# Optimization experiments

Measured on AMD Instinct MI355X. Metric: run time of the kernel, lower is better.

Reference implementation:

```python
import jax, jax.numpy as jnp
import numpy as np

NUM_HEADS = 16
EPS = 1e-6  # LinearAttention.epsilon

def setup_inputs() -> dict:
    key = jax.random.key(0)
    ks = jax.random.split(key, 10)
    B, L, D = 4, 4096, 2048
    s = 1.0 / np.sqrt(D)
    x = jax.random.normal(ks[0], (B, L, D), dtype=jnp.float32)
    attention_mask = jnp.ones((B, L), dtype=jnp.float32)
    Wq = jax.random.normal(ks[1], (D, D), dtype=jnp.float32) * s
    bq = jnp.zeros((D,), dtype=jnp.float32)
    Wk = jax.random.normal(ks[2], (D, D), dtype=jnp.float32) * s
    bk = jnp.zeros((D,), dtype=jnp.float32)
    Wv = jax.random.normal(ks[3], (D, D), dtype=jnp.float32) * s
    bv = jnp.zeros((D,), dtype=jnp.float32)
    Wo = jax.random.normal(ks[4], (D, D), dtype=jnp.float32) * s
    bo = jnp.zeros((D,), dtype=jnp.float32)
    return {"x": x, "attention_mask": attention_mask, "Wq": Wq, "bq": bq,
            "Wk": Wk, "bk": bk, "Wv": Wv, "bv": bv, "Wo": Wo, "bo": bo}

def reference(x, attention_mask, Wq, bq, Wk, bk, Wv, bv, Wo, bo):
    B, L, Dm = x.shape
    H = NUM_HEADS
    Dh = Dm // H
    # q/k/v projections -> [B, H, L, Dh]
    def proj(W, b):
        return (x @ W + b).reshape(B, L, H, Dh).transpose(0, 2, 1, 3)
    q = proj(Wq, bq)
    k = proj(Wk, bk)
    v = proj(Wv, bv)
    # feature map: elu(x) + 1
    q = jax.nn.elu(q) + 1.0
    k = jax.nn.elu(k) + 1.0
    # mask keys/values: mask [B, 1, L, 1]
    m = attention_mask[:, None, :, None]
    k = k * m
    v = v * m
    # causal linear attention via cumulative sums over sequence dim
    k_cum = jnp.cumsum(k, axis=2)          # [B,H,L,Dh]
    kv_cum = jnp.cumsum(k * v, axis=2)     # [B,H,L,Dh] (diagonal kv state, as in source)
    z = jnp.sum(q * k_cum, axis=-1) + EPS  # [B,H,L]
    z = z * attention_mask[:, None, :]
    out = (q * kv_cum) / z[..., None]      # [B,H,L,Dh]
    out = out.transpose(0, 2, 1, 3).reshape(B, L, Dm)
    return out @ Wo + bo
```

## Files before the change

kernel.cpp:

```cpp
#include <hip/hip_runtime.h>
#include <cstdint>
#include <cstddef>

#define EPS_F 1e-6f

__device__ inline unsigned short f2bf(float f) {
    union { float f; unsigned u; } v; v.f = f;
    unsigned r = v.u + 0x7fffu + ((v.u >> 16) & 1u);
    return (unsigned short)(r >> 16);
}
__device__ inline float bf2f(unsigned u16) {
    union { unsigned u; float f; } v; v.u = u16 << 16; return v.f;
}

typedef __attribute__((ext_vector_type(8))) __bf16 bf16x8;
typedef __attribute__((ext_vector_type(8))) short short8;
typedef __attribute__((ext_vector_type(8))) unsigned short ushort8;
typedef __attribute__((ext_vector_type(4))) float floatx4;
typedef __attribute__((ext_vector_type(4))) unsigned uintx4;

__device__ inline void async_load16(const void* g, void* l) {
    __builtin_amdgcn_global_load_lds((const __attribute__((address_space(1))) void*)g,
                                     (__attribute__((address_space(3))) void*)l,
                                     16, 0, 0);
}

#define LDS_OFF(p) ((unsigned)(unsigned long long)(const __attribute__((address_space(3))) void*)(p))

__global__ void cast_x_kernel(const float* __restrict__ in, unsigned short* __restrict__ out, int n8) {
    int i = blockIdx.x * blockDim.x + threadIdx.x;
    if (i < n8) {
        float4 a = ((const float4*)in)[2 * i];
        float4 b = ((const float4*)in)[2 * i + 1];
        short8 o;
        o[0] = (short)f2bf(a.x); o[1] = (short)f2bf(a.y);
        o[2] = (short)f2bf(a.z); o[3] = (short)f2bf(a.w);
        o[4] = (short)f2bf(b.x); o[5] = (short)f2bf(b.y);
        o[6] = (short)f2bf(b.z); o[7] = (short)f2bf(b.w);
        ((short8*)out)[i] = o;
    }
}

__global__ void transpose_cast_kernel(const float* __restrict__ W0, const float* __restrict__ W1,
                                      const float* __restrict__ W2, const float* __restrict__ W3,
                                      unsigned short* __restrict__ WtBase, int n) {
    const float* W = (blockIdx.z == 0) ? W0 : (blockIdx.z == 1) ? W1 : (blockIdx.z == 2) ? W2 : W3;
    unsigned short* Wt = WtBase + (size_t)blockIdx.z * n * n;
    __shared__ float tile[32][33];
    int bx = blockIdx.x * 32;
    int by = blockIdx.y * 32;
    int tx = threadIdx.x;
    int ty = threadIdx.y;
    #pragma unroll
    for (int i = 0; i < 32; i += 8)
        tile[ty + i][tx] = W[(size_t)(by + ty + i) * n + bx + tx];
    __syncthreads();
    #pragma unroll
    for (int i = 0; i < 32; i += 8)
        Wt[(size_t)(bx + ty + i) * n + by + tx] = f2bf(tile[tx][ty + i]);
}

#define BMT 256
#define BNT 256
#define BKT 32
#define SLOT_ELEMS (BMT * BKT)
#define SLOT_BYTES 16384
#define DMODEL 2048

#define DSR(dst, base, OFF) \
    asm volatile("ds_read_b128 %0, %1 offset:" OFF : "=v"(dst) : "v"(base) : "memory")
#define READ_A0(f, base) { DSR(f[0], base, "0");    DSR(f[1], base, "1024"); \
                           DSR(f[2], base, "2048"); DSR(f[3], base, "3072"); }
#define READ_A1(f, base) { DSR(f[0], base, "4096"); DSR(f[1], base, "5120"); \
                           DSR(f[2], base, "6144"); DSR(f[3], base, "7168"); }
#define READ_B(f, base)  { DSR(f[0], base, "0");    DSR(f[1], base, "1024"); \
                           DSR(f[2], base, "2048"); DSR(f[3], base, "3072"); }

#define MFMA_HALF(i0, af, bf)                                                   \
    _Pragma("unroll")                                                           \
    for (int i_ = 0; i_ < 4; i_++) {                                            \
        bf16x8 a_ = __builtin_bit_cast(bf16x8, af[i_]);                         \
        _Pragma("unroll")                                                       \
        for (int j_ = 0; j_ < 4; j_++)                                          \
            acc[i0 + i_][j_] = __builtin_amdgcn_mfma_f32_16x16x32_bf16(         \
                a_, __builtin_bit_cast(bf16x8, bf[j_]), acc[i0 + i_][j_], 0, 0, 0); \
    }

#define GEMM_ITER(T, BCUR, BNXT)                                                \
  {                                                                             \
    const int T_ = (T);                                                         \
    if (T_ <= NT - 3)      asm volatile("s_waitcnt vmcnt(4)" ::: "memory");     \
    else if (T_ == NT - 2) asm volatile("s_waitcnt vmcnt(0)" ::: "memory");     \
    __builtin_amdgcn_s_barrier();                                               \
    __builtin_amdgcn_sched_barrier(0);                                          \
    if (T_ + 3 < NT) stage(T_ + 3, (T_ + 3) & 3);                               \
    asm volatile("s_waitcnt lgkmcnt(4)" ::: "memory");                          \
    __builtin_amdgcn_sched_barrier(0);                                          \
    __builtin_amdgcn_s_setprio(1);                                              \
    MFMA_HALF(0, af0, BCUR);                                                    \
    __builtin_amdgcn_s_setprio(0);                                              \
    const int tn_ = T_ + 1;                                                     \
    const unsigned aN_ = aLane + (unsigned)((tn_ & 3) * SLOT_BYTES);            \
    const unsigned bN_ = bLane + (unsigned)((tn_ & 3) * SLOT_BYTES);            \
    if (tn_ < NT) {                                                             \
      READ_A0(af0, aN_);                                                        \
      READ_B(BNXT, bN_);                                                        \
      asm volatile("s_waitcnt lgkmcnt(8)" ::: "memory");                        \
    } else {                                                                    \
      asm volatile("s_waitcnt lgkmcnt(0)" ::: "memory");                        \
    }                                                                           \
    __builtin_amdgcn_sched_barrier(0);                                          \
    __builtin_amdgcn_s_setprio(1);                                              \
    MFMA_HALF(4, af1, BCUR);                                                    \
    __builtin_amdgcn_s_setprio(0);                                              \
    if (tn_ < NT) { READ_A1(af1, aN_); }                                        \
  }

template<int FINAL>
__global__ __launch_bounds__(512, 2)
void gemm_kernel(const unsigned short* __restrict__ A,
                 const unsigned short* __restrict__ Bt,
                 const float* __restrict__ b0, const float* __restrict__ b1,
                 const float* __restrict__ b2,
                 const float* __restrict__ mask,
                 unsigned short* __restrict__ qo, unsigned short* __restrict__ ko,
                 unsigned short* __restrict__ vo,
                 float* __restrict__ Cf,
                 int M, int K) {
    __shared__ __align__(16) unsigned short As[4 * SLOT_ELEMS];
    __shared__ __align__(16) unsigned short Bs[4 * SLOT_ELEMS];

    const int tid  = threadIdx.x;
    const int lane = tid & 63;
    const int wave = tid >> 6;
    const int wr   = wave >> 2;
    const int wc   = wave & 3;
    const int quad  = lane >> 4;
    const int row16 = lane & 15;

    const int nwg = (int)(gridDim.x * gridDim.y);
    const int bid = (int)(blockIdx.y * gridDim.x + blockIdx.x);
    const int cpx = nwg >> 3;
    const int swz = (bid & 7) * cpx + (bid >> 3);
    const int bm  = swz % (int)gridDim.x;
    const int bn  = swz / (int)gridDim.x;

    const int m0    = bm * BMT;
    const int nglob = bn * BNT;
    int mat = 0, n0 = nglob;
    const float* bias = b0;
    unsigned short* Cb = nullptr;
    if (!FINAL) {
        mat  = nglob >> 11;
        n0   = nglob & (DMODEL - 1);
        bias = (mat == 0) ? b0 : (mat == 1) ? b1 : b2;
        Cb   = (mat == 0) ? qo : (mat == 1) ? ko : vo;
    }

    floatx4 acc[8][4] = {};

    const unsigned short* gA[2];
    const unsigned short* gB[2];
    #pragma unroll
    for (int b = 0; b < 2; b++) {
        int s = b * 512 + tid;
        int r = s >> 2, c = s & 3;
        int cg = c ^ ((r >> 1) & 3);
        gA[b] = A  + (size_t)(m0 + r) * K + cg * 8;
        gB[b] = Bt + (size_t)(nglob + r) * K + cg * 8;
    }

    const unsigned asB = LDS_OFF(As);
    const unsigned bsB = LDS_OFF(Bs);
    const unsigned cP    = (unsigned)(quad ^ ((row16 >> 1) & 3));
    const unsigned aLane = asB + (unsigned)(wr * 8192 + row16 * 64) + cP * 16u;
    const unsigned bLane = bsB + (unsigned)(wc * 4096 + row16 * 64) + cP * 16u;

    auto stage = [&](int tt, int sl) {
        const int koff = tt * BKT;
        #pragma unroll
        for (int b = 0; b < 2; b++) {
            int s = b * 512 + tid;
            async_load16(gA[b] + koff, As + sl * SLOT_ELEMS + s * 8);
            async_load16(gB[b] + koff, Bs + sl * SLOT_ELEMS + s * 8);
        }
    };

    const int NT = K / BKT;
    stage(0, 0); stage(1, 1); stage(2, 2);
    asm volatile("s_waitcnt vmcnt(8)" ::: "memory");
    __builtin_amdgcn_s_barrier();
    __builtin_amdgcn_sched_barrier(0);

    uintx4 af0[4], af1[4], bfE[4], bfO[4];
    READ_A0(af0, aLane);
    READ_B(bfE, bLane);
    READ_A1(af1, aLane);

    for (int t = 0; t < NT; t += 2) {
        GEMM_ITER(t,     bfE, bfO);
        GEMM_ITER(t + 1, bfO, bfE);
    }

    float bcache[4];
    #pragma unroll
    for (int j = 0; j < 4; j++) bcache[j] = bias[n0 + wc * 64 + j * 16 + row16];
    #pragma unroll
    for (int i = 0; i < 8; i++) {
        #pragma unroll
        for (int r = 0; r < 4; r++) {
            int row = m0 + wr * 128 + i * 16 + quad * 4 + r;
            float mr = 1.0f;
            if (!FINAL && mat >= 1) mr = mask[row];
            #pragma unroll
            for (int j = 0; j < 4; j++) {
                int col = n0 + wc * 64 + j * 16 + row16;
                float v = acc[i][j][r] + bcache[j];
                if (FINAL) {
                    Cf[(size_t)row * DMODEL + col] = v;
                } else {
                    if (mat <= 1) v = (v > 0.f) ? (v + 1.f) : __expf(v);
                    v *= mr;
                    Cb[(size_t)row * DMODEL + col] = f2bf(v);
                }
            }
        }
    }
}

#define SL    4096
#define SD    2048
#define SH    16
#define CHUNK 64
#define NCH   64

__global__ void scan_partial_kernel(const unsigned short* __restrict__ k,
                                    const unsigned short* __restrict__ v,
                                    float* __restrict__ sumK, float* __restrict__ sumKV) {
    int blk = blockIdx.x;
    int c = blk & (NCH - 1), bh = blk >> 6;
    int b = bh >> 4, h = bh & (SH - 1);
    int lane = threadIdx.x;
    int tg = lane >> 4, dg = lane & 15;
    size_t base = ((size_t)(b * SL + c * CHUNK + tg)) * SD + h * 128 + dg * 8;
    float sk[8] = {0.f, 0.f, 0.f, 0.f, 0.f, 0.f, 0.f, 0.f};
    float skv[8] = {0.f, 0.f, 0.f, 0.f, 0.f, 0.f, 0.f, 0.f};
    for (int it = 0; it < CHUNK / 4; it++) {
        ushort8 kw = *(const ushort8*)(k + base);
        ushort8 vw = *(const ushort8*)(v + base);
        #pragma unroll
        for (int j = 0; j < 8; j++) {
            float kf = bf2f(kw[j]);
            float vf = bf2f(vw[j]);
            sk[j] += kf; skv[j] += kf * vf;
        }
        base += (size_t)4 * SD;
    }
    #pragma unroll
    for (int j = 0; j < 8; j++) {
        sk[j]  += __shfl_xor(sk[j], 16);  sk[j]  += __shfl_xor(sk[j], 32);
        skv[j] += __shfl_xor(skv[j], 16); skv[j] += __shfl_xor(skv[j], 32);
    }
    if (tg == 0) {
        size_t o = ((size_t)bh * NCH + c) * 128 + dg * 8;
        *(float4*)(sumK  + o)     = make_float4(sk[0], sk[1], sk[2], sk[3]);
        *(float4*)(sumK  + o + 4) = make_float4(sk[4], sk[5], sk[6], sk[7]);
        *(float4*)(sumKV + o)     = make_float4(skv[0], skv[1], skv[2], skv[3]);
        *(float4*)(sumKV + o + 4) = make_float4(skv[4], skv[5], skv[6], skv[7]);
    }
}

__global__ void scan_offsets_kernel(const float* __restrict__ sumK, const float* __restrict__ sumKV,
                                    float* __restrict__ offK, float* __restrict__ offKV) {
    int bh = blockIdx.x;
    int d  = threadIdx.x;
    float aK = 0.f, aKV = 0.f;
    for (int c = 0; c < NCH; c++) {
        size_t o = ((size_t)bh * NCH + c) * 128 + d;
        float sk = sumK[o], skv = sumKV[o];
        offK[o] = aK; offKV[o] = aKV;
        aK += sk; aKV += skv;
    }
}

__global__ void scan_final_kernel(const unsigned short* __restrict__ q,
                                  const unsigned short* __restrict__ k,
                                  const unsigned short* __restrict__ v,
                                  const float* __restrict__ offK, const float* __restrict__ offKV,
                                  const float* __restrict__ mask,
                                  unsigned short* __restrict__ out) {
    int blk = blockIdx.x;
    int c = blk & (NCH - 1), bh = blk >> 6;
    int b = bh >> 4, h = bh & (SH - 1);
    int lane = threadIdx.x;
    size_t ob = ((size_t)bh * NCH + c) * 128 + 2 * lane;
    float2 kcv = *(const float2*)(offK  + ob);
    float2 kvv = *(const float2*)(offKV + ob);
    float kc0 = kcv.x, kc1 = kcv.y, kv0 = kvv.x, kv1 = kvv.y;
    size_t base = ((size_t)(b * SL + c * CHUNK)) * SD + h * 128 + 2 * lane;
    const float* mrow = mask + (size_t)b * SL + c * CHUNK;
    for (int s = 0; s < CHUNK / 4; s++) {
        unsigned kw[4], vw[4], qw[4];
        #pragma unroll
        for (int u = 0; u < 4; u++) {
            size_t a = base + (size_t)u * SD;
            kw[u] = *(const unsigned*)(k + a);
            vw[u] = *(const unsigned*)(v + a);
            qw[u] = *(const unsigned*)(q + a);
        }
        float p[4], n0[4], n1[4];
        #pragma unroll
        for (int u = 0; u < 4; u++) {
            float kk0 = bf2f(kw[u] & 0xffff), kk1 = bf2f(kw[u] >> 16);
            float vv0 = bf2f(vw[u] & 0xffff), vv1 = bf2f(vw[u] >> 16);
            float qq0 = bf2f(qw[u] & 0xffff), qq1 = bf2f(qw[u] >> 16);
            kc0 += kk0; kc1 += kk1;
            kv0 += kk0 * vv0; kv1 += kk1 * vv1;
            p[u]  = qq0 * kc0 + qq1 * kc1;
            n0[u] = qq0 * kv0; n1[u] = qq1 * kv1;
        }
        #pragma unroll
        for (int off = 32; off > 0; off >>= 1) {
            #pragma unroll
            for (int u = 0; u < 4; u++) p[u] += __shfl_xor(p[u], off);
        }
        #pragma unroll
        for (int u = 0; u < 4; u++) {
            float z = (p[u] + EPS_F) * mrow[s * 4 + u];
            float inv = 1.0f / z;
            unsigned o0 = f2bf(n0[u] * inv);
            unsigned o1 = f2bf(n1[u] * inv);
            *(unsigned*)(out + base + (size_t)u * SD) = o0 | (o1 << 16);
        }
        base += (size_t)4 * SD;
    }
}

extern "C" void kernel_launch(void* const* d_in, const int* in_sizes, int n_in,
                              void* d_out, int out_size, void* d_ws, size_t ws_size,
                              hipStream_t stream) {
    const float* x  = (const float*)d_in[0];
    const float* am = (const float*)d_in[1];
    const float* Wq = (const float*)d_in[2];
    const float* bq = (const float*)d_in[3];
    const float* Wk = (const float*)d_in[4];
    const float* bk = (const float*)d_in[5];
    const float* Wv = (const float*)d_in[6];
    const float* bv = (const float*)d_in[7];
    const float* Wo = (const float*)d_in[8];
    const float* bo = (const float*)d_in[9];
    float* out = (float*)d_out;

    const int Bb = 4, L = 4096, D = 2048;
    const int M = Bb * L;
    const size_t MD = (size_t)M * D;

    char* w = (char*)d_ws;
    unsigned short* xb    = (unsigned short*)w; w += MD * 2;
    unsigned short* qb    = (unsigned short*)w; w += MD * 2;
    unsigned short* kb    = (unsigned short*)w; w += MD * 2;
    unsigned short* vb    = (unsigned short*)w; w += MD * 2;
    unsigned short* WT    = (unsigned short*)w; w += (size_t)4 * D * D * 2;
    float* sumK  = (float*)w; w += (size_t)64 * NCH * 128 * 4;
    float* sumKV = (float*)w; w += (size_t)64 * NCH * 128 * 4;
    float* offK  = (float*)w; w += (size_t)64 * NCH * 128 * 4;
    float* offKV = (float*)w; w += (size_t)64 * NCH * 128 * 4;
    unsigned short* attnb = xb;

    int n8 = (int)(MD / 8);
    cast_x_kernel<<<(n8 + 255) / 256, 256, 0, stream>>>(x, xb, n8);
    dim3 tb(32, 8);
    dim3 tg(D / 32, D / 32, 4);
    transpose_cast_kernel<<<tg, tb, 0, stream>>>(Wq, Wk, Wv, Wo, WT, D);

    dim3 gq(M / BMT, 3 * D / BNT);
    gemm_kernel<0><<<gq, 512, 0, stream>>>(xb, WT, bq, bk, bv, am, qb, kb, vb, nullptr, M, D);

    scan_partial_kernel<<<64 * NCH, 64, 0, stream>>>(kb, vb, sumK, sumKV);
    scan_offsets_kernel<<<64, 128, 0, stream>>>(sumK, sumKV, offK, offKV);
    scan_final_kernel<<<64 * NCH, 64, 0, stream>>>(qb, kb, vb, offK, offKV, am, attnb);

    dim3 go(M / BMT, D / BNT);
    gemm_kernel<1><<<go, 512, 0, stream>>>(attnb, WT + (size_t)3 * D * D, bo, nullptr, nullptr,
                                           nullptr, nullptr, nullptr, nullptr, out, M, D);
}
```

Before: 889.2 us.

## Restructure GEMM main loop into barrier-phased split A/B staging pipeline

Measured after the change: 904.2 us. Within noise of the previous version (+1.7%).

```diff
diff --git a/kernel.cpp b/kernel.cpp
--- a/kernel.cpp
+++ b/kernel.cpp
@@ -85,36 +85,6 @@
             acc[i0 + i_][j_] = __builtin_amdgcn_mfma_f32_16x16x32_bf16(         \
                 a_, __builtin_bit_cast(bf16x8, bf[j_]), acc[i0 + i_][j_], 0, 0, 0); \
     }
-
-#define GEMM_ITER(T, BCUR, BNXT)                                                \
-  {                                                                             \
-    const int T_ = (T);                                                         \
-    if (T_ <= NT - 3)      asm volatile("s_waitcnt vmcnt(4)" ::: "memory");     \
-    else if (T_ == NT - 2) asm volatile("s_waitcnt vmcnt(0)" ::: "memory");     \
-    __builtin_amdgcn_s_barrier();                                               \
-    __builtin_amdgcn_sched_barrier(0);                                          \
-    if (T_ + 3 < NT) stage(T_ + 3, (T_ + 3) & 3);                               \
-    asm volatile("s_waitcnt lgkmcnt(4)" ::: "memory");                          \
-    __builtin_amdgcn_sched_barrier(0);                                          \
-    __builtin_amdgcn_s_setprio(1);                                              \
-    MFMA_HALF(0, af0, BCUR);                                                    \
-    __builtin_amdgcn_s_setprio(0);                                              \
-    const int tn_ = T_ + 1;                                                     \
-    const unsigned aN_ = aLane + (unsigned)((tn_ & 3) * SLOT_BYTES);            \
-    const unsigned bN_ = bLane + (unsigned)((tn_ & 3) * SLOT_BYTES);            \
-    if (tn_ < NT) {                                                             \
-      READ_A0(af0, aN_);                                                        \
-      READ_B(BNXT, bN_);                                                        \
-      asm volatile("s_waitcnt lgkmcnt(8)" ::: "memory");                        \
-    } else {                                                                    \
-      asm volatile("s_waitcnt lgkmcnt(0)" ::: "memory");                        \
-    }                                                                           \
-    __builtin_amdgcn_sched_barrier(0);                                          \
-    __builtin_amdgcn_s_setprio(1);                                              \
-    MFMA_HALF(4, af1, BCUR);                                                    \
-    __builtin_amdgcn_s_setprio(0);                                              \
-    if (tn_ < NT) { READ_A1(af1, aN_); }                                        \
-  }
 
 template<int FINAL>
 __global__ __launch_bounds__(512, 2)
@@ -176,31 +146,55 @@
     const unsigned aLane = asB + (unsigned)(wr * 8192 + row16 * 64) + cP * 16u;
     const unsigned bLane = bsB + (unsigned)(wc * 4096 + row16 * 64) + cP * 16u;
 
-    auto stage = [&](int tt, int sl) {
-        const int koff = tt * BKT;
-        #pragma unroll
-        for (int b = 0; b < 2; b++) {
-            int s = b * 512 + tid;
-            async_load16(gA[b] + koff, As + sl * SLOT_ELEMS + s * 8);
-            async_load16(gB[b] + koff, Bs + sl * SLOT_ELEMS + s * 8);
-        }
+    auto stageA = [&](int S) {
+        const int koff = S * BKT;
+        const int sl   = S & 3;
+        #pragma unroll
+        for (int b = 0; b < 2; b++)
+            async_load16(gA[b] + koff, As + sl * SLOT_ELEMS + (b * 512 + tid) * 8);
     };
+    auto stageB = [&](int S) {
+        const int koff = S * BKT;
+        const int sl   = S & 3;
+        #pragma unroll
+        for (int b = 0; b < 2; b++)
+            async_load16(gB[b] + koff, Bs + sl * SLOT_ELEMS + (b * 512 + tid) * 8);
+    };
 
     const int NT = K / BKT;
-    stage(0, 0); stage(1, 1); stage(2, 2);
-    asm volatile("s_waitcnt vmcnt(8)" ::: "memory");
+    stageA(0); stageB(0); stageA(1); stageB(1);
+    asm volatile("s_waitcnt vmcnt(4)" ::: "memory");
     __builtin_amdgcn_s_barrier();
     __builtin_amdgcn_sched_barrier(0);
 
-    uintx4 af0[4], af1[4], bfE[4], bfO[4];
-    READ_A0(af0, aLane);
-    READ_B(bfE, bLane);
-    READ_A1(af1, aLane);
-
-    for (int t = 0; t < NT; t += 2) {
-        GEMM_ITER(t,     bfE, bfO);
-        GEMM_ITER(t + 1, bfO, bfE);
-    }
+    uintx4 af0[4], af1[4], bf[4];
+
+    for (int S = 0; S < NT; ++S) {
+        const unsigned aOff = aLane + (unsigned)((S & 3) * SLOT_BYTES);
+        const unsigned bOff = bLane + (unsigned)((S & 3) * SLOT_BYTES);
+        READ_A0(af0, aOff);
+        READ_B(bf, bOff);
+        if (S + 2 < NT) stageA(S + 2);
+        __builtin_amdgcn_s_barrier();
+        asm volatile("s_waitcnt lgkmcnt(0)" ::: "memory");
+        __builtin_amdgcn_sched_barrier(0);
+        __builtin_amdgcn_s_setprio(1);
+        MFMA_HALF(0, af0, bf);
+        __builtin_amdgcn_s_setprio(0);
+        __builtin_amdgcn_s_barrier();
+        READ_A1(af1, aOff);
+        if (S + 2 < NT) stageB(S + 2);
+        if (S < NT - 2)       asm volatile("s_waitcnt vmcnt(4)" ::: "memory");
+        else if (S == NT - 2) asm volatile("s_waitcnt vmcnt(0)" ::: "memory");
+        __builtin_amdgcn_s_barrier();
+        asm volatile("s_waitcnt lgkmcnt(0)" ::: "memory");
+        __builtin_amdgcn_sched_barrier(0);
+        __builtin_amdgcn_s_setprio(1);
+        MFMA_HALF(4, af1, bf);
+        __builtin_amdgcn_s_setprio(0);
+        __builtin_amdgcn_s_barrier();
+    }
+    __builtin_amdgcn_sched_barrier(0);
 
     float bcache[4];
     #pragma unroll
```
